# Kernel optimization log

Measured on AMD Instinct MI355X. Metric: run time of the kernel, lower is better.

Reference implementation:

```python
import jax, jax.numpy as jnp
import numpy as np

WS = 6      # window_size
SS = 3      # shift_size
NH = 8      # num_heads
DIM = 384
HD = DIM // NH
SCALE = HD ** -0.5


def _window_mask(H, W):
    # region ids: [:ss,:ss]=0, [:ss,ss:]=1, [ss:,:ss]=2, [ss:,ss:]=3
    row = (jnp.arange(H) >= SS).astype(jnp.int32)
    col = (jnp.arange(W) >= SS).astype(jnp.int32)
    region = row[:, None] * 2 + col[None, :]            # (H, W)
    region = jnp.roll(region, (-SS, -SS), axis=(0, 1))
    ids = region.reshape(H // WS, WS, W // WS, WS).transpose(0, 2, 1, 3)
    ids = ids.reshape(-1, WS * WS)                      # (nW, V)
    eq = ids[:, :, None] == ids[:, None, :]             # (nW, V, V)
    return jnp.where(eq, 0.0, -jnp.inf).astype(jnp.float32)


def setup_inputs():
    key = jax.random.key(0)
    k = jax.random.split(key, 5)
    B, H, W, D = 32, 48, 48, DIM
    return {
        "x": jax.random.normal(k[0], (B, H, W, D), jnp.float32),
        "w_qkv": jax.random.normal(k[1], (D, 3 * D), jnp.float32) * 0.02,
        "b_qkv": jax.random.normal(k[2], (3 * D,), jnp.float32) * 0.02,
        "w_proj": jax.random.normal(k[3], (D, D), jnp.float32) * 0.02,
        "b_proj": jax.random.normal(k[4], (D,), jnp.float32) * 0.02,
    }


def reference(x, w_qkv, b_qkv, w_proj, b_proj):
    B, H, W, D = x.shape
    nWh, nWw = H // WS, W // WS
    nW, V = nWh * nWw, WS * WS

    x = jnp.roll(x, (-SS, -SS), axis=(1, 2))
    amask = _window_mask(H, W)                          # (nW, V, V)

    # window partition -> (B*nW, V, D)
    xw = x.reshape(B, nWh, WS, nWw, WS, D).transpose(0, 1, 3, 2, 4, 5)
    xw = xw.reshape(B * nW, V, D)

    qkv = xw @ w_qkv + b_qkv                            # (M, V, 3D)
    qkv = qkv.reshape(B * nW, V, 3, NH, HD).transpose(2, 0, 3, 1, 4)
    q, k, v = qkv[0], qkv[1], qkv[2]                    # (M, NH, V, HD)

    scores = jnp.einsum("mhvd,mhud->mhvu", q, k) * SCALE
    scores = scores.reshape(B, nW, NH, V, V) + amask[None, :, None]
    attn = jax.nn.softmax(scores, axis=-1).reshape(B * nW, NH, V, V)

    out = jnp.einsum("mhvu,mhud->mhvd", attn, v)        # (M, NH, V, HD)
    out = out.transpose(0, 2, 1, 3).reshape(B * nW, V, D)

    # window reverse -> (B, H, W, D)
    out = out.reshape(B, nWh, nWw, WS, WS, D).transpose(0, 1, 3, 2, 4, 5)
    out = out.reshape(B, H, W, D)
    out = jnp.roll(out, (SS, SS), axis=(1, 2))
    return out @ w_proj + b_proj
```

## Files before the change

### kernel.cpp

```cpp
#include <hip/hip_runtime.h>
#include <hip/hip_bf16.h>

namespace {

constexpr int Bn   = 32;
constexpr int IMG  = 48;
constexpr int Dm   = 384;
constexpr int NHn  = 8;
constexpr int WSn  = 6;
constexpr int NWn  = 64;
constexpr int Mn   = Bn * NWn;
constexpr int Vn   = 36;
constexpr int ROWS = Mn * Vn;
constexpr int K3   = 3 * Dm;
constexpr int HEADS_E = Vn * 48;
constexpr float SCALE = 0.14433756729740643f;

using short8 = __attribute__((ext_vector_type(8))) short;
using f32x4  = __attribute__((ext_vector_type(4))) float;

__device__ __forceinline__ float bf2f(unsigned short u) {
    return __uint_as_float(((unsigned)u) << 16);
}
__device__ __forceinline__ unsigned short f2bf(float f) {
    unsigned u = __float_as_uint(f);
    u += 0x7FFFu + ((u >> 16) & 1u);
    return (unsigned short)(u >> 16);
}

__device__ __forceinline__ int invol(int f) {
    return (f & 56) | ((f ^ (f >> 3)) & 7);
}

__device__ __forceinline__ void gl_lds16(const unsigned short* g, unsigned short* l) {
    __builtin_amdgcn_global_load_lds(
        (const __attribute__((address_space(1))) unsigned int*)g,
        (__attribute__((address_space(3))) unsigned int*)l, 16, 0, 0);
}

__device__ __forceinline__ int gather_base(int row) {
    int m = row / Vn, v = row - m * Vn;
    int b = m >> 6, w = m & 63;
    int wh = w >> 3, ww = w & 7;
    int gh = wh * WSn + v / WSn;
    int gw = ww * WSn + v % WSn;
    int fi = (gh + 3) % IMG;
    int fj = (gw + 3) % IMG;
    return ((b * IMG + fi) * IMG + fj) * Dm;
}

__device__ __forceinline__ int region_id(int t, int wh, int ww) {
    int hi = (wh == 7) ? ((t / 6) < 3) : 1;
    int lo = (ww == 7) ? ((t % 6) < 3) : 1;
    return (hi << 1) | lo;
}

__global__ __launch_bounds__(256)
void gather_x(const float* __restrict__ x, unsigned short* __restrict__ xg)
{
    int idx = blockIdx.x * 256 + threadIdx.x;
    int row = idx / 96;
    int c4  = (idx - row * 96) * 4;
    float4 v = *(const float4*)(x + (size_t)gather_base(row) + c4);
    ushort4 o;
    o.x = f2bf(v.x); o.y = f2bf(v.y); o.z = f2bf(v.z); o.w = f2bf(v.w);
    *(ushort4*)(xg + (size_t)row * Dm + c4) = o;
}

__global__ __launch_bounds__(256)
void prep_w(const float* __restrict__ wq, const float* __restrict__ wp,
            unsigned short* __restrict__ wqT, unsigned short* __restrict__ wpT)
{
    int idx = blockIdx.x * 256 + threadIdx.x;
    if (idx < K3 * Dm) {
        int n = idx / Dm, k = idx - n * Dm;
        wqT[idx] = f2bf(wq[(size_t)k * K3 + n]);
    } else {
        int i2 = idx - K3 * Dm;
        if (i2 < Dm * Dm) {
            int n = i2 / Dm, k = i2 - n * Dm;
            wpT[i2] = f2bf(wp[(size_t)k * Dm + n]);
        }
    }
}

__global__ __launch_bounds__(256)
void qkv_mfma(const unsigned short* __restrict__ xg,
              const unsigned short* __restrict__ wqT,
              const float* __restrict__ bq,
              unsigned short* __restrict__ qh,
              unsigned short* __restrict__ kh,
              unsigned short* __restrict__ vh)
{
    __shared__ __align__(16) unsigned short As[3][128 * 32];
    __shared__ __align__(16) unsigned short Bs[3][128 * 32];

    const int tid  = threadIdx.x;
    const int wave = tid >> 6, lane = tid & 63;
    const int quad = lane >> 4, l15 = lane & 15;
    const int id = (blockIdx.x & 7) * 648 + (blockIdx.x >> 3);
    const int nT = id % (K3 / 128);
    const int mT = id / (K3 / 128);
    const int rowA0 = mT * 128, rowB0 = nT * 128;

    const int fS  = invol(lane);
    const int rS  = fS >> 2;
    const int kcS = (fS & 3) * 8;
    const unsigned short* gA = xg  + (size_t)(rowA0 + wave * 32 + rS) * Dm + kcS;
    const unsigned short* gB = wqT + (size_t)(rowB0 + wave * 32 + rS) * Dm + kcS;

    const int wm = wave >> 1, wn = wave & 1;
    int aoff[4], boff[4];
#pragma unroll
    for (int i = 0; i < 4; i++) {
        int R = wm * 64 + i * 16 + l15;
        aoff[i] = (R >> 4) * 512 + invol((R & 15) * 4 + quad) * 8;
        int S = wn * 64 + i * 16 + l15;
        boff[i] = (S >> 4) * 512 + invol((S & 15) * 4 + quad) * 8;
    }

    f32x4 acc[4][4];
#pragma unroll
    for (int i = 0; i < 4; i++)
#pragma unroll
        for (int j = 0; j < 4; j++) acc[i][j] = (f32x4){0.f, 0.f, 0.f, 0.f};

    auto STAGE = [&](int buf, int k0) {
        gl_lds16(gA + k0,           &As[buf][(wave * 32) * 32]);
        gl_lds16(gA + 16 * Dm + k0, &As[buf][(wave * 32 + 16) * 32]);
        gl_lds16(gB + k0,           &Bs[buf][(wave * 32) * 32]);
        gl_lds16(gB + 16 * Dm + k0, &Bs[buf][(wave * 32 + 16) * 32]);
    };
    auto COMPUTE = [&](int buf) {
        short8 af[4], bfr[4];
#pragma unroll
        for (int i = 0; i < 4; i++) af[i]  = *(const short8*)&As[buf][aoff[i]];
#pragma unroll
        for (int j = 0; j < 4; j++) bfr[j] = *(const short8*)&Bs[buf][boff[j]];
#pragma unroll
        for (int i = 0; i < 4; i++)
#pragma unroll
            for (int j = 0; j < 4; j++)
                acc[i][j] = __builtin_amdgcn_mfma_f32_16x16x32_bf16(af[i], bfr[j], acc[i][j], 0, 0, 0);
    };

    STAGE(0, 0);
    STAGE(1, 32);
#pragma unroll
    for (int t = 0; t < 10; ++t) {
        asm volatile("s_waitcnt vmcnt(4)" ::: "memory");
        __builtin_amdgcn_s_barrier();
        STAGE((t + 2) % 3, (t + 2) * 32);
        COMPUTE(t % 3);
    }
    asm volatile("s_waitcnt vmcnt(4)" ::: "memory");
    __builtin_amdgcn_s_barrier();
    COMPUTE(10 % 3);
    asm volatile("s_waitcnt vmcnt(0)" ::: "memory");
    __builtin_amdgcn_s_barrier();
    COMPUTE(11 % 3);

    unsigned short* outb = (nT < 3) ? qh : (nT < 6) ? kh : vh;
    const int csub = (nT < 3) ? 0 : (nT < 6) ? 384 : 768;
#pragma unroll
    for (int j = 0; j < 4; j++) {
        int col = rowB0 + wn * 64 + j * 16 + l15;
        float b = bq[col];
        int c  = col - csub;
        int hh = c / 48, dd = c - hh * 48;
#pragma unroll
        for (int i = 0; i < 4; i++) {
#pragma unroll
            for (int r = 0; r < 4; r++) {
                int row = rowA0 + wm * 64 + i * 16 + quad * 4 + r;
                int mm = row / 36, vv = row - mm * 36;
                outb[((size_t)(mm * 8 + hh) * 36 + vv) * 48 + dd] = f2bf(acc[i][j][r] + b);
            }
        }
    }
}

__global__ __launch_bounds__(256)
void attn_mfma(const unsigned short* __restrict__ qh,
               const unsigned short* __restrict__ kh,
               const unsigned short* __restrict__ vh,
               unsigned short* __restrict__ att)
{
    __shared__ __align__(16) unsigned short Pl[4][48 * 56];
    __shared__ __align__(16) unsigned short Vt[4][48 * 64];

    const int tid  = threadIdx.x;
    const int wave = tid >> 6, lane = tid & 63;
    const int quad = lane >> 4, l15 = lane & 15;
    const int W = blockIdx.x * 4 + wave;
    const int m = W >> 3, h = W & 7;
    const int w = m & 63, wh = w >> 3, ww = w & 7;
    const bool need_mask = (wh == 7) || (ww == 7);

    const short8 zf = {0, 0, 0, 0, 0, 0, 0, 0};

    {
        short8* vz = (short8*)&Vt[0][0];
#pragma unroll
        for (int z = 0; z < 6; z++) vz[z * 256 + tid] = zf;
    }
    __syncthreads();

    const size_t hb = (size_t)(m * 8 + h) * HEADS_E;

    const unsigned short* qb = qh + hb;
    const unsigned short* kb = kh + hb;
    short8 qf[3][2], kf[3][2];
#pragma unroll
    for (int t = 0; t < 3; t++) {
        const unsigned short* qr = qb + (t * 16 + l15) * 48;
        qf[t][0] = *(const short8*)(qr + quad * 8);
        qf[t][1] = (quad < 2) ? *(const short8*)(qr + 32 + quad * 8) : zf;
        const unsigned short* kr = kb + (t * 16 + l15) * 48;
        kf[t][0] = *(const short8*)(kr + quad * 8);
        kf[t][1] = *(const short8*)(kr + 32 + quad * 8);
    }

    unsigned short* vws = &Vt[wave][0];
    {
        const unsigned short* vb = vh + hb;
#pragma unroll
        for (int p = 0; p < 4; p++) {
            int c = p * 64 + lane;
            if (c < 216) {
                short8 vv = *(const short8*)(vb + c * 8);
                int v  = c / 6, d0 = (c - v * 6) * 8;
                int g  = v >> 3, v7 = v & 7;
#pragma unroll
                for (int jj = 0; jj < 8; jj++) {
                    int d = d0 + jj;
                    int slot = (g + (d & 7) + (d >> 3)) & 7;
                    vws[d * 64 + slot * 8 + v7] = (unsigned short)vv[jj];
                }
            }
        }
    }

    f32x4 acc[3][3];
#pragma unroll
    for (int i = 0; i < 3; i++)
#pragma unroll
        for (int j = 0; j < 3; j++) acc[i][j] = (f32x4){0.f, 0.f, 0.f, 0.f};
    __builtin_amdgcn_s_setprio(1);
#pragma unroll
    for (int i = 0; i < 3; i++)
#pragma unroll
        for (int j = 0; j < 3; j++) {
            acc[i][j] = __builtin_amdgcn_mfma_f32_16x16x32_bf16(qf[i][0], kf[j][0], acc[i][j], 0, 0, 0);
            acc[i][j] = __builtin_amdgcn_mfma_f32_16x16x32_bf16(qf[i][1], kf[j][1], acc[i][j], 0, 0, 0);
        }
    __builtin_amdgcn_s_setprio(0);

#pragma unroll
    for (int i = 0; i < 3; i++) {
        float rs[4] = {0.f, 0.f, 0.f, 0.f};
        if (need_mask) {
#pragma unroll
            for (int j = 0; j < 3; j++) {
                int C = j * 16 + l15;
                int idc = region_id(C, wh, ww);
#pragma unroll
                for (int r = 0; r < 4; r++) {
                    int R = i * 16 + quad * 4 + r;
                    int idr = region_id(R, wh, ww);
                    float s = acc[i][j][r] * SCALE;
                    s = (C >= 36 || idr != idc) ? -1e30f : fminf(s, 30.f);
                    float e = __expf(s);
                    acc[i][j][r] = e;
                    rs[r] += e;
                }
            }
        } else {
#pragma unroll
            for (int j = 0; j < 3; j++) {
                int C = j * 16 + l15;
#pragma unroll
                for (int r = 0; r < 4; r++) {
                    float s = acc[i][j][r] * SCALE;
                    s = (C >= 36) ? -1e30f : fminf(s, 30.f);
                    float e = __expf(s);
                    acc[i][j][r] = e;
                    rs[r] += e;
                }
            }
        }
#pragma unroll
        for (int r = 0; r < 4; r++) {
#pragma unroll
            for (int d = 1; d < 16; d <<= 1) rs[r] += __shfl_xor(rs[r], d, 16);
            rs[r] = 1.f / rs[r];
        }
#pragma unroll
        for (int j = 0; j < 3; j++)
#pragma unroll
            for (int r = 0; r < 4; r++) {
                int R = i * 16 + quad * 4 + r;
                int C = j * 16 + l15;
                Pl[wave][R * 56 + C] = f2bf(acc[i][j][r] * rs[r]);
            }
    }
    __syncthreads();

    short8 pf[3][2], vf[3][2];
#pragma unroll
    for (int t = 0; t < 3; t++) {
        const unsigned short* pr = &Pl[wave][(t * 16 + l15) * 56];
        pf[t][0] = *(const short8*)(pr + quad * 8);
        pf[t][1] = (quad < 2) ? *(const short8*)(pr + 32 + quad * 8) : zf;
        int d  = t * 16 + l15;
        int sb = (d & 7) + (d >> 3);
        vf[t][0] = *(const short8*)(vws + d * 64 + (((quad + sb) & 7) * 8));
        vf[t][1] = *(const short8*)(vws + d * 64 + (((quad + 4 + sb) & 7) * 8));
    }
    f32x4 oacc[3][3];
#pragma unroll
    for (int i = 0; i < 3; i++)
#pragma unroll
        for (int j = 0; j < 3; j++) oacc[i][j] = (f32x4){0.f, 0.f, 0.f, 0.f};
    __builtin_amdgcn_s_setprio(1);
#pragma unroll
    for (int i = 0; i < 3; i++)
#pragma unroll
        for (int j = 0; j < 3; j++) {
            oacc[i][j] = __builtin_amdgcn_mfma_f32_16x16x32_bf16(pf[i][0], vf[j][0], oacc[i][j], 0, 0, 0);
            oacc[i][j] = __builtin_amdgcn_mfma_f32_16x16x32_bf16(pf[i][1], vf[j][1], oacc[i][j], 0, 0, 0);
        }
    __builtin_amdgcn_s_setprio(0);

#pragma unroll
    for (int i = 0; i < 3; i++)
#pragma unroll
        for (int r = 0; r < 4; r++) {
            int R = i * 16 + quad * 4 + r;
            if (R < 36) {
#pragma unroll
                for (int j = 0; j < 3; j++)
                    att[((size_t)m * 36 + R) * Dm + h * 48 + j * 16 + l15] = f2bf(oacc[i][j][r]);
            }
        }
}

__global__ __launch_bounds__(256)
void proj_mfma(const unsigned short* __restrict__ att,
               const unsigned short* __restrict__ wpT,
               const float* __restrict__ bp,
               float* __restrict__ out)
{
    __shared__ __align__(16) unsigned short As[3][128 * 32];
    __shared__ __align__(16) unsigned short Bs[3][128 * 32];
    __shared__ int rowOut[128];

    const int tid  = threadIdx.x;
    const int wave = tid >> 6, lane = tid & 63;
    const int quad = lane >> 4, l15 = lane & 15;
    const int id = (blockIdx.x & 7) * 216 + (blockIdx.x >> 3);
    const int nT = id % (Dm / 128);
    const int mT = id / (Dm / 128);
    const int rowA0 = mT * 128, rowB0 = nT * 128;

    if (tid < 128) rowOut[tid] = gather_base(rowA0 + tid);

    const int fS  = invol(lane);
    const int rS  = fS >> 2;
    const int kcS = (fS & 3) * 8;
    const unsigned short* gA = att + (size_t)(rowA0 + wave * 32 + rS) * Dm + kcS;
    const unsigned short* gB = wpT + (size_t)(rowB0 + wave * 32 + rS) * Dm + kcS;

    const int wm = wave >> 1, wn = wave & 1;
    int aoff[4], boff[4];
#pragma unroll
    for (int i = 0; i < 4; i++) {
        int R = wm * 64 + i * 16 + l15;
        aoff[i] = (R >> 4) * 512 + invol((R & 15) * 4 + quad) * 8;
        int S = wn * 64 + i * 16 + l15;
        boff[i] = (S >> 4) * 512 + invol((S & 15) * 4 + quad) * 8;
    }

    f32x4 acc[4][4];
#pragma unroll
    for (int i = 0; i < 4; i++)
#pragma unroll
        for (int j = 0; j < 4; j++) acc[i][j] = (f32x4){0.f, 0.f, 0.f, 0.f};

    auto STAGE = [&](int buf, int k0) {
        gl_lds16(gA + k0,           &As[buf][(wave * 32) * 32]);
        gl_lds16(gA + 16 * Dm + k0, &As[buf][(wave * 32 + 16) * 32]);
        gl_lds16(gB + k0,           &Bs[buf][(wave * 32) * 32]);
        gl_lds16(gB + 16 * Dm + k0, &Bs[buf][(wave * 32 + 16) * 32]);
    };
    auto COMPUTE = [&](int buf) {
        short8 af[4], bfr[4];
#pragma unroll
        for (int i = 0; i < 4; i++) af[i]  = *(const short8*)&As[buf][aoff[i]];
#pragma unroll
        for (int j = 0; j < 4; j++) bfr[j] = *(const short8*)&Bs[buf][boff[j]];
#pragma unroll
        for (int i = 0; i < 4; i++)
#pragma unroll
            for (int j = 0; j < 4; j++)
                acc[i][j] = __builtin_amdgcn_mfma_f32_16x16x32_bf16(af[i], bfr[j], acc[i][j], 0, 0, 0);
    };

    STAGE(0, 0);
    STAGE(1, 32);
#pragma unroll
    for (int t = 0; t < 10; ++t) {
        asm volatile("s_waitcnt vmcnt(4)" ::: "memory");
        __builtin_amdgcn_s_barrier();
        STAGE((t + 2) % 3, (t + 2) * 32);
        COMPUTE(t % 3);
    }
    asm volatile("s_waitcnt vmcnt(4)" ::: "memory");
    __builtin_amdgcn_s_barrier();
    COMPUTE(10 % 3);
    asm volatile("s_waitcnt vmcnt(0)" ::: "memory");
    __builtin_amdgcn_s_barrier();
    COMPUTE(11 % 3);

#pragma unroll
    for (int j = 0; j < 4; j++) {
        int col = rowB0 + wn * 64 + j * 16 + l15;
        float b = bp[col];
#pragma unroll
        for (int i = 0; i < 4; i++) {
#pragma unroll
            for (int r = 0; r < 4; r++) {
                int lrow = wm * 64 + i * 16 + quad * 4 + r;
                out[(size_t)rowOut[lrow] + col] = acc[i][j][r] + b;
            }
        }
    }
}

}

extern "C" void kernel_launch(void* const* d_in, const int* in_sizes, int n_in,
                              void* d_out, int out_size, void* d_ws, size_t ws_size,
                              hipStream_t stream)
{
    const float* x  = (const float*)d_in[0];
    const float* wq = (const float*)d_in[1];
    const float* bq = (const float*)d_in[2];
    const float* wp = (const float*)d_in[3];
    const float* bp = (const float*)d_in[4];
    float* out = (float*)d_out;

    const size_t HE   = (size_t)Mn * NHn * HEADS_E;
    const size_t XG_E = (size_t)ROWS * Dm;
    unsigned short* qh  = (unsigned short*)d_ws;
    unsigned short* kh  = qh + HE;
    unsigned short* vh  = kh + HE;
    unsigned short* xg  = vh + HE;
    unsigned short* att = xg;
    unsigned short* wqT = xg + XG_E;
    unsigned short* wpT = wqT + (size_t)K3 * Dm;

    prep_w   <<<(K3 * Dm + Dm * Dm + 255) / 256, 256, 0, stream>>>(wq, wp, wqT, wpT);
    gather_x <<<ROWS * (Dm / 4) / 256,            256, 0, stream>>>(x, xg);
    qkv_mfma <<<(ROWS / 128) * (K3 / 128),        256, 0, stream>>>(xg, wqT, bq, qh, kh, vh);
    attn_mfma<<<(Mn * NHn) / 4,                   256, 0, stream>>>(qh, kh, vh, att);
    proj_mfma<<<(ROWS / 128) * (Dm / 128),        256, 0, stream>>>(att, wpT, bp, out);
}
```

Baseline: 422.2 us.

## Fuse window attention with output projection in one kernel per window

Merges the attention kernel and the projection GEMM into one kernel where each block handles one window: 4 waves each compute 2 heads, stage the 36x384 attention output in LDS in the swizzled layout the MFMA expects, then multiply by the projection weights read directly from global memory. This removes the bf16 att round trip through global memory and one kernel launch. In exchange, each block reads the whole 384x384 projection weight from global/L2 without LDS staging, the M tile is only 36 rows (padded to 48), so MFMA utilisation drops, and only 2048 blocks run with sequential per-head work.

```diff
diff --git a/kernel.cpp b/kernel.cpp
--- a/kernel.cpp
+++ b/kernel.cpp
@@ -181,260 +181,231 @@
 }
 
 __global__ __launch_bounds__(256)
-void attn_mfma(const unsigned short* __restrict__ qh,
+void attn_proj(const unsigned short* __restrict__ qh,
                const unsigned short* __restrict__ kh,
                const unsigned short* __restrict__ vh,
-               unsigned short* __restrict__ att)
-{
-    __shared__ __align__(16) unsigned short Pl[4][48 * 56];
-    __shared__ __align__(16) unsigned short Vt[4][48 * 64];
-
-    const int tid  = threadIdx.x;
-    const int wave = tid >> 6, lane = tid & 63;
-    const int quad = lane >> 4, l15 = lane & 15;
-    const int W = blockIdx.x * 4 + wave;
-    const int m = W >> 3, h = W & 7;
-    const int w = m & 63, wh = w >> 3, ww = w & 7;
-    const bool need_mask = (wh == 7) || (ww == 7);
-
-    const short8 zf = {0, 0, 0, 0, 0, 0, 0, 0};
-
-    {
-        short8* vz = (short8*)&Vt[0][0];
-#pragma unroll
-        for (int z = 0; z < 6; z++) vz[z * 256 + tid] = zf;
-    }
-    __syncthreads();
-
-    const size_t hb = (size_t)(m * 8 + h) * HEADS_E;
-
-    const unsigned short* qb = qh + hb;
-    const unsigned short* kb = kh + hb;
-    short8 qf[3][2], kf[3][2];
-#pragma unroll
-    for (int t = 0; t < 3; t++) {
-        const unsigned short* qr = qb + (t * 16 + l15) * 48;
-        qf[t][0] = *(const short8*)(qr + quad * 8);
-        qf[t][1] = (quad < 2) ? *(const short8*)(qr + 32 + quad * 8) : zf;
-        const unsigned short* kr = kb + (t * 16 + l15) * 48;
-        kf[t][0] = *(const short8*)(kr + quad * 8);
-        kf[t][1] = *(const short8*)(kr + 32 + quad * 8);
-    }
-
-    unsigned short* vws = &Vt[wave][0];
-    {
-        const unsigned short* vb = vh + hb;
-#pragma unroll
-        for (int p = 0; p < 4; p++) {
-            int c = p * 64 + lane;
-            if (c < 216) {
-                short8 vv = *(const short8*)(vb + c * 8);
-                int v  = c / 6, d0 = (c - v * 6) * 8;
-                int g  = v >> 3, v7 = v & 7;
-#pragma unroll
-                for (int jj = 0; jj < 8; jj++) {
-                    int d = d0 + jj;
-                    int slot = (g + (d & 7) + (d >> 3)) & 7;
-                    vws[d * 64 + slot * 8 + v7] = (unsigned short)vv[jj];
-                }
-            }
-        }
-    }
-
-    f32x4 acc[3][3];
-#pragma unroll
-    for (int i = 0; i < 3; i++)
-#pragma unroll
-        for (int j = 0; j < 3; j++) acc[i][j] = (f32x4){0.f, 0.f, 0.f, 0.f};
-    __builtin_amdgcn_s_setprio(1);
-#pragma unroll
-    for (int i = 0; i < 3; i++)
-#pragma unroll
-        for (int j = 0; j < 3; j++) {
-            acc[i][j] = __builtin_amdgcn_mfma_f32_16x16x32_bf16(qf[i][0], kf[j][0], acc[i][j], 0, 0, 0);
-            acc[i][j] = __builtin_amdgcn_mfma_f32_16x16x32_bf16(qf[i][1], kf[j][1], acc[i][j], 0, 0, 0);
-        }
-    __builtin_amdgcn_s_setprio(0);
-
-#pragma unroll
-    for (int i = 0; i < 3; i++) {
-        float rs[4] = {0.f, 0.f, 0.f, 0.f};
-        if (need_mask) {
-#pragma unroll
-            for (int j = 0; j < 3; j++) {
-                int C = j * 16 + l15;
-                int idc = region_id(C, wh, ww);
-#pragma unroll
-                for (int r = 0; r < 4; r++) {
-                    int R = i * 16 + quad * 4 + r;
-                    int idr = region_id(R, wh, ww);
-                    float s = acc[i][j][r] * SCALE;
-                    s = (C >= 36 || idr != idc) ? -1e30f : fminf(s, 30.f);
-                    float e = __expf(s);
-                    acc[i][j][r] = e;
-                    rs[r] += e;
-                }
-            }
-        } else {
-#pragma unroll
-            for (int j = 0; j < 3; j++) {
-                int C = j * 16 + l15;
-#pragma unroll
-                for (int r = 0; r < 4; r++) {
-                    float s = acc[i][j][r] * SCALE;
-                    s = (C >= 36) ? -1e30f : fminf(s, 30.f);
-                    float e = __expf(s);
-                    acc[i][j][r] = e;
-                    rs[r] += e;
-                }
-            }
-        }
-#pragma unroll
-        for (int r = 0; r < 4; r++) {
-#pragma unroll
-            for (int d = 1; d < 16; d <<= 1) rs[r] += __shfl_xor(rs[r], d, 16);
-            rs[r] = 1.f / rs[r];
-        }
-#pragma unroll
-        for (int j = 0; j < 3; j++)
-#pragma unroll
-            for (int r = 0; r < 4; r++) {
-                int R = i * 16 + quad * 4 + r;
-                int C = j * 16 + l15;
-                Pl[wave][R * 56 + C] = f2bf(acc[i][j][r] * rs[r]);
-            }
-    }
-    __syncthreads();
-
-    short8 pf[3][2], vf[3][2];
-#pragma unroll
-    for (int t = 0; t < 3; t++) {
-        const unsigned short* pr = &Pl[wave][(t * 16 + l15) * 56];
-        pf[t][0] = *(const short8*)(pr + quad * 8);
-        pf[t][1] = (quad < 2) ? *(const short8*)(pr + 32 + quad * 8) : zf;
-        int d  = t * 16 + l15;
-        int sb = (d & 7) + (d >> 3);
-        vf[t][0] = *(const short8*)(vws + d * 64 + (((quad + sb) & 7) * 8));
-        vf[t][1] = *(const short8*)(vws + d * 64 + (((quad + 4 + sb) & 7) * 8));
-    }
-    f32x4 oacc[3][3];
-#pragma unroll
-    for (int i = 0; i < 3; i++)
-#pragma unroll
-        for (int j = 0; j < 3; j++) oacc[i][j] = (f32x4){0.f, 0.f, 0.f, 0.f};
-    __builtin_amdgcn_s_setprio(1);
-#pragma unroll
-    for (int i = 0; i < 3; i++)
-#pragma unroll
-        for (int j = 0; j < 3; j++) {
-            oacc[i][j] = __builtin_amdgcn_mfma_f32_16x16x32_bf16(pf[i][0], vf[j][0], oacc[i][j], 0, 0, 0);
-            oacc[i][j] = __builtin_amdgcn_mfma_f32_16x16x32_bf16(pf[i][1], vf[j][1], oacc[i][j], 0, 0, 0);
-        }
-    __builtin_amdgcn_s_setprio(0);
-
-#pragma unroll
-    for (int i = 0; i < 3; i++)
-#pragma unroll
-        for (int r = 0; r < 4; r++) {
-            int R = i * 16 + quad * 4 + r;
-            if (R < 36) {
-#pragma unroll
-                for (int j = 0; j < 3; j++)
-                    att[((size_t)m * 36 + R) * Dm + h * 48 + j * 16 + l15] = f2bf(oacc[i][j][r]);
-            }
-        }
-}
-
-__global__ __launch_bounds__(256)
-void proj_mfma(const unsigned short* __restrict__ att,
                const unsigned short* __restrict__ wpT,
                const float* __restrict__ bp,
                float* __restrict__ out)
 {
-    __shared__ __align__(16) unsigned short As[3][128 * 32];
-    __shared__ __align__(16) unsigned short Bs[3][128 * 32];
-    __shared__ int rowOut[128];
+    __shared__ __align__(16) unsigned short SMEM[23040];
+    __shared__ int rowOut36[36];
 
     const int tid  = threadIdx.x;
     const int wave = tid >> 6, lane = tid & 63;
     const int quad = lane >> 4, l15 = lane & 15;
-    const int id = (blockIdx.x & 7) * 216 + (blockIdx.x >> 3);
-    const int nT = id % (Dm / 128);
-    const int mT = id / (Dm / 128);
-    const int rowA0 = mT * 128, rowB0 = nT * 128;
-
-    if (tid < 128) rowOut[tid] = gather_base(rowA0 + tid);
-
-    const int fS  = invol(lane);
-    const int rS  = fS >> 2;
-    const int kcS = (fS & 3) * 8;
-    const unsigned short* gA = att + (size_t)(rowA0 + wave * 32 + rS) * Dm + kcS;
-    const unsigned short* gB = wpT + (size_t)(rowB0 + wave * 32 + rS) * Dm + kcS;
-
-    const int wm = wave >> 1, wn = wave & 1;
-    int aoff[4], boff[4];
-#pragma unroll
-    for (int i = 0; i < 4; i++) {
-        int R = wm * 64 + i * 16 + l15;
-        aoff[i] = (R >> 4) * 512 + invol((R & 15) * 4 + quad) * 8;
-        int S = wn * 64 + i * 16 + l15;
-        boff[i] = (S >> 4) * 512 + invol((S & 15) * 4 + quad) * 8;
-    }
-
-    f32x4 acc[4][4];
-#pragma unroll
-    for (int i = 0; i < 4; i++)
-#pragma unroll
-        for (int j = 0; j < 4; j++) acc[i][j] = (f32x4){0.f, 0.f, 0.f, 0.f};
-
-    auto STAGE = [&](int buf, int k0) {
-        gl_lds16(gA + k0,           &As[buf][(wave * 32) * 32]);
-        gl_lds16(gA + 16 * Dm + k0, &As[buf][(wave * 32 + 16) * 32]);
-        gl_lds16(gB + k0,           &Bs[buf][(wave * 32) * 32]);
-        gl_lds16(gB + 16 * Dm + k0, &Bs[buf][(wave * 32 + 16) * 32]);
-    };
-    auto COMPUTE = [&](int buf) {
-        short8 af[4], bfr[4];
-#pragma unroll
-        for (int i = 0; i < 4; i++) af[i]  = *(const short8*)&As[buf][aoff[i]];
-#pragma unroll
-        for (int j = 0; j < 4; j++) bfr[j] = *(const short8*)&Bs[buf][boff[j]];
-#pragma unroll
-        for (int i = 0; i < 4; i++)
-#pragma unroll
-            for (int j = 0; j < 4; j++)
-                acc[i][j] = __builtin_amdgcn_mfma_f32_16x16x32_bf16(af[i], bfr[j], acc[i][j], 0, 0, 0);
-    };
-
-    STAGE(0, 0);
-    STAGE(1, 32);
-#pragma unroll
-    for (int t = 0; t < 10; ++t) {
-        asm volatile("s_waitcnt vmcnt(4)" ::: "memory");
-        __builtin_amdgcn_s_barrier();
-        STAGE((t + 2) % 3, (t + 2) * 32);
-        COMPUTE(t % 3);
-    }
-    asm volatile("s_waitcnt vmcnt(4)" ::: "memory");
-    __builtin_amdgcn_s_barrier();
-    COMPUTE(10 % 3);
-    asm volatile("s_waitcnt vmcnt(0)" ::: "memory");
-    __builtin_amdgcn_s_barrier();
-    COMPUTE(11 % 3);
-
-#pragma unroll
-    for (int j = 0; j < 4; j++) {
-        int col = rowB0 + wn * 64 + j * 16 + l15;
-        float b = bp[col];
-#pragma unroll
-        for (int i = 0; i < 4; i++) {
+    const int m = blockIdx.x;
+    const int w = m & 63, wh = w >> 3, ww = w & 7;
+    const bool need_mask = (wh == 7) || (ww == 7);
+
+    if (tid < 36) rowOut36[tid] = gather_base(m * 36 + tid);
+
+    unsigned short* Plw = SMEM + wave * 2688;
+    unsigned short* vws = SMEM + 10752 + wave * 3072;
+
+    const short8 zf = {0, 0, 0, 0, 0, 0, 0, 0};
+
+    {
+        short8* vz = (short8*)(SMEM + 10752);
+#pragma unroll
+        for (int z = 0; z < 6; z++) vz[z * 256 + tid] = zf;
+    }
+    __syncthreads();
+
+    f32x4 oacc2[2][3][3];
+
+#pragma unroll
+    for (int hi = 0; hi < 2; hi++) {
+        const int h = wave * 2 + hi;
+        const size_t hb = (size_t)(m * 8 + h) * HEADS_E;
+
+        const unsigned short* qb = qh + hb;
+        const unsigned short* kb = kh + hb;
+        short8 qf[3][2], kf[3][2];
+#pragma unroll
+        for (int t = 0; t < 3; t++) {
+            const unsigned short* qr = qb + (t * 16 + l15) * 48;
+            qf[t][0] = *(const short8*)(qr + quad * 8);
+            qf[t][1] = (quad < 2) ? *(const short8*)(qr + 32 + quad * 8) : zf;
+            const unsigned short* kr = kb + (t * 16 + l15) * 48;
+            kf[t][0] = *(const short8*)(kr + quad * 8);
+            kf[t][1] = *(const short8*)(kr + 32 + quad * 8);
+        }
+
+        {
+            const unsigned short* vb = vh + hb;
+#pragma unroll
+            for (int p = 0; p < 4; p++) {
+                int c = p * 64 + lane;
+                if (c < 216) {
+                    short8 vv = *(const short8*)(vb + c * 8);
+                    int v  = c / 6, d0 = (c - v * 6) * 8;
+                    int g  = v >> 3, v7 = v & 7;
+#pragma unroll
+                    for (int jj = 0; jj < 8; jj++) {
+                        int d = d0 + jj;
+                        int slot = (g + (d & 7) + (d >> 3)) & 7;
+                        vws[d * 64 + slot * 8 + v7] = (unsigned short)vv[jj];
+                    }
+                }
+            }
+        }
+
+        f32x4 sacc[3][3];
+#pragma unroll
+        for (int i = 0; i < 3; i++)
+#pragma unroll
+            for (int j = 0; j < 3; j++) sacc[i][j] = (f32x4){0.f, 0.f, 0.f, 0.f};
+        __builtin_amdgcn_s_setprio(1);
+#pragma unroll
+        for (int i = 0; i < 3; i++)
+#pragma unroll
+            for (int j = 0; j < 3; j++) {
+                sacc[i][j] = __builtin_amdgcn_mfma_f32_16x16x32_bf16(qf[i][0], kf[j][0], sacc[i][j], 0, 0, 0);
+                sacc[i][j] = __builtin_amdgcn_mfma_f32_16x16x32_bf16(qf[i][1], kf[j][1], sacc[i][j], 0, 0, 0);
+            }
+        __builtin_amdgcn_s_setprio(0);
+
+#pragma unroll
+        for (int i = 0; i < 3; i++) {
+            float rs[4] = {0.f, 0.f, 0.f, 0.f};
+            if (need_mask) {
+#pragma unroll
+                for (int j = 0; j < 3; j++) {
+                    int C = j * 16 + l15;
+                    int idc = region_id(C, wh, ww);
+#pragma unroll
+                    for (int r = 0; r < 4; r++) {
+                        int R = i * 16 + quad * 4 + r;
+                        int idr = region_id(R, wh, ww);
+                        float s = sacc[i][j][r] * SCALE;
+                        s = (C >= 36 || idr != idc) ? -1e30f : fminf(s, 30.f);
+                        float e = __expf(s);
+                        sacc[i][j][r] = e;
+                        rs[r] += e;
+                    }
+                }
+            } else {
+#pragma unroll
+                for (int j = 0; j < 3; j++) {
+                    int C = j * 16 + l15;
+#pragma unroll
+                    for (int r = 0; r < 4; r++) {
+                        float s = sacc[i][j][r] * SCALE;
+                        s = (C >= 36) ? -1e30f : fminf(s, 30.f);
+                        float e = __expf(s);
+                        sacc[i][j][r] = e;
+                        rs[r] += e;
+                    }
+                }
+            }
 #pragma unroll
             for (int r = 0; r < 4; r++) {
-                int lrow = wm * 64 + i * 16 + quad * 4 + r;
-                out[(size_t)rowOut[lrow] + col] = acc[i][j][r] + b;
-            }
-        }
-    }
+#pragma unroll
+                for (int d = 1; d < 16; d <<= 1) rs[r] += __shfl_xor(rs[r], d, 16);
+                rs[r] = 1.f / rs[r];
+            }
+#pragma unroll
+            for (int j = 0; j < 3; j++)
+#pragma unroll
+                for (int r = 0; r < 4; r++) {
+                    int R = i * 16 + quad * 4 + r;
+                    int C = j * 16 + l15;
+                    Plw[R * 56 + C] = f2bf(sacc[i][j][r] * rs[r]);
+                }
+        }
+        __syncthreads();
+
+        short8 pf[3][2], vf[3][2];
+#pragma unroll
+        for (int t = 0; t < 3; t++) {
+            const unsigned short* pr = &Plw[(t * 16 + l15) * 56];
+            pf[t][0] = *(const short8*)(pr + quad * 8);
+            pf[t][1] = (quad < 2) ? *(const short8*)(pr + 32 + quad * 8) : zf;
+            int d  = t * 16 + l15;
+            int sb = (d & 7) + (d >> 3);
+            vf[t][0] = *(const short8*)(vws + d * 64 + (((quad + sb) & 7) * 8));
+            vf[t][1] = *(const short8*)(vws + d * 64 + (((quad + 4 + sb) & 7) * 8));
+        }
+#pragma unroll
+        for (int i = 0; i < 3; i++)
+#pragma unroll
+            for (int j = 0; j < 3; j++) oacc2[hi][i][j] = (f32x4){0.f, 0.f, 0.f, 0.f};
+        __builtin_amdgcn_s_setprio(1);
+#pragma unroll
+        for (int i = 0; i < 3; i++)
+#pragma unroll
+            for (int j = 0; j < 3; j++) {
+                oacc2[hi][i][j] = __builtin_amdgcn_mfma_f32_16x16x32_bf16(pf[i][0], vf[j][0], oacc2[hi][i][j], 0, 0, 0);
+                oacc2[hi][i][j] = __builtin_amdgcn_mfma_f32_16x16x32_bf16(pf[i][1], vf[j][1], oacc2[hi][i][j], 0, 0, 0);
+            }
+        __builtin_amdgcn_s_setprio(0);
+    }
+
+    __syncthreads();
+
+#pragma unroll
+    for (int hi = 0; hi < 2; hi++) {
+        const int h = wave * 2 + hi;
+#pragma unroll
+        for (int i = 0; i < 3; i++)
+#pragma unroll
+            for (int r = 0; r < 4; r++) {
+                int R = i * 16 + quad * 4 + r;
+                if (R < 36) {
+                    int band = R >> 4, f4 = (R & 15) * 4;
+#pragma unroll
+                    for (int j = 0; j < 3; j++) {
+                        int k  = h * 48 + j * 16 + l15;
+                        int ks = k >> 5, kk = k & 31;
+                        SMEM[(ks * 3 + band) * 512 + invol(f4 + (kk >> 3)) * 8 + (kk & 7)]
+                            = f2bf(oacc2[hi][i][j][r]);
+                    }
+                }
+            }
+    }
+    __syncthreads();
+
+    const int aoffP = invol(l15 * 4 + quad) * 8;
+    const unsigned short* gBp = wpT + (size_t)(wave * 96 + l15) * 384 + quad * 8;
+    f32x4 pacc[3][6];
+#pragma unroll
+    for (int i = 0; i < 3; i++)
+#pragma unroll
+        for (int j = 0; j < 6; j++) pacc[i][j] = (f32x4){0.f, 0.f, 0.f, 0.f};
+
+#pragma unroll
+    for (int ks = 0; ks < 12; ks++) {
+        short8 bfr[6];
+#pragma unroll
+        for (int j = 0; j < 6; j++)
+            bfr[j] = *(const short8*)(gBp + (size_t)j * 16 * 384 + ks * 32);
+        short8 af[3];
+#pragma unroll
+        for (int i = 0; i < 3; i++)
+            af[i] = *(const short8*)&SMEM[(ks * 3 + i) * 512 + aoffP];
+#pragma unroll
+        for (int i = 0; i < 3; i++)
+#pragma unroll
+            for (int j = 0; j < 6; j++)
+                pacc[i][j] = __builtin_amdgcn_mfma_f32_16x16x32_bf16(af[i], bfr[j], pacc[i][j], 0, 0, 0);
+    }
+
+    float bpv[6];
+#pragma unroll
+    for (int j = 0; j < 6; j++) bpv[j] = bp[wave * 96 + j * 16 + l15];
+#pragma unroll
+    for (int i = 0; i < 3; i++)
+#pragma unroll
+        for (int r = 0; r < 4; r++) {
+            int R = i * 16 + quad * 4 + r;
+            if (R < 36) {
+                float* orow = out + rowOut36[R];
+#pragma unroll
+                for (int j = 0; j < 6; j++)
+                    orow[wave * 96 + j * 16 + l15] = pacc[i][j][r] + bpv[j];
+            }
+        }
 }
 
 }
@@ -456,13 +427,11 @@
     unsigned short* kh  = qh + HE;
     unsigned short* vh  = kh + HE;
     unsigned short* xg  = vh + HE;
-    unsigned short* att = xg;
     unsigned short* wqT = xg + XG_E;
     unsigned short* wpT = wqT + (size_t)K3 * Dm;
 
     prep_w   <<<(K3 * Dm + Dm * Dm + 255) / 256, 256, 0, stream>>>(wq, wp, wqT, wpT);
     gather_x <<<ROWS * (Dm / 4) / 256,            256, 0, stream>>>(x, xg);
     qkv_mfma <<<(ROWS / 128) * (K3 / 128),        256, 0, stream>>>(xg, wqT, bq, qh, kh, vh);
-    attn_mfma<<<(Mn * NHn) / 4,                   256, 0, stream>>>(qh, kh, vh, att);
-    proj_mfma<<<(ROWS / 128) * (Dm / 128),        256, 0, stream>>>(att, wpT, bp, out);
-}
+    attn_proj<<<Mn,                               256, 0, stream>>>(qh, kh, vh, wpT, bp, out);
+}
```

New measurement: 442.5 us. +4.8%, slower.
